# Kernel optimization log

Measured on AMD Instinct MI355X. Metric: run time of the kernel, lower is better.

The kernel has to match this reference:

```python
import jax, jax.numpy as jnp
import numpy as np

B, T, N, NIN = 2, 10, 128, 6
K, H = 4, 128          # edge_types, n_hid
E = N * (N - 1)        # fully-connected, no self-loops


def _linear_init(key, out_f, in_f, bias=True):
    k1, k2 = jax.random.split(key)
    bound = 1.0 / np.sqrt(in_f)
    W = jax.random.uniform(k1, (out_f, in_f), jnp.float32, -bound, bound)
    if bias:
        b = jax.random.uniform(k2, (out_f,), jnp.float32, -bound, bound)
        return W, b
    return W


def setup_inputs() -> dict:
    key = jax.random.key(0)
    ks = jax.random.split(key, 20)
    # graph structure: one-hot receiver/sender matrices (NRI style)
    off_diag = np.ones((N, N), dtype=np.float32) - np.eye(N, dtype=np.float32)
    send_idx, recv_idx = np.where(off_diag)
    eye = np.eye(N, dtype=np.float32)
    rel_rec = jnp.asarray(eye[recv_idx])   # [E, N]
    rel_send = jnp.asarray(eye[send_idx])  # [E, N]

    data = jax.random.normal(ks[0], (B, T, N, NIN), jnp.float32)
    rel_type = jax.nn.softmax(jax.random.normal(ks[1], (B, E, K), jnp.float32), axis=-1)

    # per-edge-type message MLPs, stacked over edge type
    m1 = [_linear_init(ks[2 + i], H, 2 * H) for i in range(K)]
    m2 = [_linear_init(ks[6 + i], H, H) for i in range(K)]
    W_msg1 = jnp.stack([w for w, _ in m1]); b_msg1 = jnp.stack([b for _, b in m1])
    W_msg2 = jnp.stack([w for w, _ in m2]); b_msg2 = jnp.stack([b for _, b in m2])

    W_hr = _linear_init(ks[10], H, H, bias=False)
    W_hi = _linear_init(ks[11], H, H, bias=False)
    W_hh = _linear_init(ks[12], H, H, bias=False)
    W_ir, b_ir = _linear_init(ks[13], H, NIN)
    W_ii, b_ii = _linear_init(ks[14], H, NIN)
    W_in, b_in = _linear_init(ks[15], H, NIN)
    W_o1, b_o1 = _linear_init(ks[16], H, H)
    W_o2, b_o2 = _linear_init(ks[17], H, H)
    W_o3, b_o3 = _linear_init(ks[18], NIN, H)

    return dict(data=data, rel_type=rel_type, rel_rec=rel_rec, rel_send=rel_send,
                W_msg1=W_msg1, b_msg1=b_msg1, W_msg2=W_msg2, b_msg2=b_msg2,
                W_hr=W_hr, W_hi=W_hi, W_hh=W_hh,
                W_ir=W_ir, b_ir=b_ir, W_ii=W_ii, b_ii=b_ii, W_in=W_in, b_in=b_in,
                W_o1=W_o1, b_o1=b_o1, W_o2=W_o2, b_o2=b_o2, W_o3=W_o3, b_o3=b_o3)


def reference(data, rel_type, rel_rec, rel_send,
              W_msg1, b_msg1, W_msg2, b_msg2,
              W_hr, W_hi, W_hh,
              W_ir, b_ir, W_ii, b_ii, W_in, b_in,
              W_o1, b_o1, W_o2, b_o2, W_o3, b_o3):
    norm = float(K)  # skip_first=False -> all edge types, norm = edge_types
    rel_type_k = jnp.transpose(rel_type, (2, 0, 1))[..., None]  # [K, B, E, 1]

    def single_step(hidden, ins):
        # gather node hidden states to edges
        receivers = jnp.einsum('en,bnh->beh', rel_rec, hidden)
        senders = jnp.einsum('en,bnh->beh', rel_send, hidden)
        pre_msg = jnp.concatenate([receivers, senders], axis=-1)  # [B, E, 2H]
        # per-edge-type 2-layer tanh MLP, batched over edge types (dropout p=0)
        msg = jnp.tanh(jnp.einsum('bef,khf->kbeh', pre_msg, W_msg1) + b_msg1[:, None, None, :])
        msg = jnp.tanh(jnp.einsum('kbeh,kgh->kbeg', msg, W_msg2) + b_msg2[:, None, None, :])
        all_msgs = jnp.sum(msg * rel_type_k, axis=0) / norm      # [B, E, H]
        # scatter-aggregate edge messages to receiver nodes
        agg = jnp.einsum('beh,en->bnh', all_msgs, rel_rec) / NIN  # [B, N, H]
        # GRU-style update
        r = jax.nn.sigmoid(ins @ W_ir.T + b_ir + agg @ W_hr.T)
        i = jax.nn.sigmoid(ins @ W_ii.T + b_ii + agg @ W_hi.T)
        n = jnp.tanh(ins @ W_in.T + b_in + r * (agg @ W_hh.T))
        hidden_new = (1.0 - i) * n + i * hidden
        # output MLP with residual (dropout p=0)
        p = jax.nn.relu(hidden_new @ W_o1.T + b_o1)
        p = jax.nn.relu(p @ W_o2.T + b_o2)
        pred = ins + p @ W_o3.T + b_o3
        return hidden_new, pred

    hidden0 = jnp.zeros((B, N, H), data.dtype)
    # pred_steps=1 (default) -> every step consumes the ground-truth frame
    ins_seq = jnp.transpose(data[:, :-1], (1, 0, 2, 3))  # [T-1, B, N, NIN]
    _, preds = jax.lax.scan(single_step, hidden0, ins_seq)
    # stack(dim=1).transpose(1,2) -> [B, N, T-1, NIN]
    return jnp.transpose(preds, (1, 2, 0, 3))
```

## Files before the change

### kernel.cpp

```cpp
#include <hip/hip_runtime.h>

#define NN 128
#define HH 128
#define BB 2
#define KT 4
#define EE 16256
#define TT 9

typedef __bf16 v8bf __attribute__((ext_vector_type(8)));
typedef float v4f __attribute__((ext_vector_type(4)));

__device__ __forceinline__ float tanh_fast(float x) {
  return 1.0f - __fdividef(2.0f, __expf(2.0f * x) + 1.0f);
}
__device__ __forceinline__ float sigmoid_fast(float x) {
  return __fdividef(1.0f, 1.0f + __expf(-x));
}
__device__ __forceinline__ unsigned short f2bf(float f) {
  unsigned int u = __float_as_uint(f);
  u += 0x7FFFu + ((u >> 16) & 1u);
  return (unsigned short)(u >> 16);
}

__global__ void prep_kernel(const float* __restrict__ W_msg1,
                            const float* __restrict__ W_msg2,
                            const float* __restrict__ rel_type,
                            unsigned short* __restrict__ W1hi,
                            unsigned short* __restrict__ W1lo,
                            unsigned short* __restrict__ W2bf,
                            float* __restrict__ relp) {
  int idx = blockIdx.x * 256 + threadIdx.x;
  {
    int h = idx & 127, g = (idx >> 7) & 127, ku = idx >> 14;
    int k = ku >> 1, u = ku & 1;
    float w = W_msg1[(k * 128 + g) * 256 + u * 128 + h];
    unsigned short hi = f2bf(w);
    float whi = __uint_as_float(((unsigned int)hi) << 16);
    W1hi[idx] = hi;
    W1lo[idx] = f2bf(w - whi);
  }
  if (idx < 65536) W2bf[idx] = f2bf(W_msg2[idx]);
  {
    int r = idx & 127, k = (idx >> 7) & 3, n = (idx >> 9) & 127, b = idx >> 16;
    float v = 0.f;
    if (r != n) {
      int e = r * 127 + (n < r ? n : n - 1);
      v = rel_type[(b * EE + e) * KT + k];
    }
    relp[idx] = v;
  }
}

__global__ __launch_bounds__(512)
void step_kernel(const float* __restrict__ data,
                 const float* __restrict__ b_msg1,
                 const float* __restrict__ b_msg2,
                 const float* __restrict__ W_hr,
                 const float* __restrict__ W_hi_,
                 const float* __restrict__ W_hh,
                 const float* __restrict__ W_ir, const float* __restrict__ b_ir,
                 const float* __restrict__ W_ii, const float* __restrict__ b_ii,
                 const float* __restrict__ W_in, const float* __restrict__ b_in,
                 const float* __restrict__ W_o1, const float* __restrict__ b_o1,
                 const float* __restrict__ W_o2, const float* __restrict__ b_o2,
                 const float* __restrict__ W_o3, const float* __restrict__ b_o3,
                 const unsigned short* __restrict__ W1hi,
                 const unsigned short* __restrict__ W1lo,
                 const unsigned short* __restrict__ W2bf,
                 const float* __restrict__ relp,
                 float* __restrict__ hidden,
                 const float* __restrict__ UVin,
                 float* __restrict__ UVout,
                 float* __restrict__ outp,
                 int t) {
  __shared__ unsigned short w2_lds[65536];
  __shared__ float ub_lds[512];
  __shared__ float b2_lds[512];
  __shared__ float rel_lds[512];
  __shared__ float colsum[8][128];
  __shared__ float agg_lds[128];
  __shared__ float hid_lds[128];
  __shared__ float hn_lds[128];
  __shared__ float ins_lds[6];
  __shared__ float g_r[128], g_i[128], g_hh[128], g_in[128];
  __shared__ float p1_lds[128], p2_lds[128];

  const int tid = threadIdx.x;
  const int lane = tid & 63;
  const int wave = tid >> 6;
  const int b = blockIdx.x >> 7;
  const int n = blockIdx.x & 127;

  {
    const uint4* w2g = (const uint4*)W2bf;
#pragma unroll
    for (int i = 0; i < 16; ++i) {
      int cid = tid + i * 512;
      int plane = cid >> 11, c2 = cid & 2047;
      int g = c2 >> 4, cc = c2 & 15;
      uint4 v = w2g[cid];
      int off = (plane << 15) + (g << 8) + (cc << 4);
      off ^= (g & 7) << 4;
      *(uint4*)((char*)w2_lds + off) = v;
    }
    int k = tid >> 7, h = tid & 127;
    ub_lds[tid] = UVin[(((k * 2 + 0) * BB + b) * NN + n) * HH + h] + b_msg1[tid];
    b2_lds[tid] = b_msg2[tid];
    rel_lds[tid] = relp[(b * NN + n) * (KT * NN) + tid];
  }
  __syncthreads();

  float acc_all[8][4];
#pragma unroll
  for (int c = 0; c < 8; ++c)
#pragma unroll
    for (int r = 0; r < 4; ++r) acc_all[c][r] = 0.f;

  for (int k = 0; k < KT; ++k) {
    const float* vbase = UVin + (((k * 2 + 1) * BB + b) * NN + (wave * 16 + (lane & 15))) * HH;
    v8bf af[4];
#pragma unroll
    for (int ks = 0; ks < 4; ++ks) {
      int c0 = ks * 32 + ((lane >> 4) << 3);
      float4 v0 = *(const float4*)(vbase + c0);
      float4 v1 = *(const float4*)(vbase + c0 + 4);
      const float* up = ub_lds + k * 128 + c0;
      float4 u0 = *(const float4*)(up);
      float4 u1 = *(const float4*)(up + 4);
      af[ks][0] = (__bf16)tanh_fast(u0.x + v0.x);
      af[ks][1] = (__bf16)tanh_fast(u0.y + v0.y);
      af[ks][2] = (__bf16)tanh_fast(u0.z + v0.z);
      af[ks][3] = (__bf16)tanh_fast(u0.w + v0.w);
      af[ks][4] = (__bf16)tanh_fast(u1.x + v1.x);
      af[ks][5] = (__bf16)tanh_fast(u1.y + v1.y);
      af[ks][6] = (__bf16)tanh_fast(u1.z + v1.z);
      af[ks][7] = (__bf16)tanh_fast(u1.w + v1.w);
    }
    v4f acck[8];
#pragma unroll
    for (int c = 0; c < 8; ++c) acck[c] = (v4f){0.f, 0.f, 0.f, 0.f};
#pragma unroll
    for (int ks = 0; ks < 4; ++ks) {
#pragma unroll
      for (int c = 0; c < 8; ++c) {
        int g = c * 16 + (lane & 15);
        int boff = (k << 15) + (g << 8) + (ks << 6) + ((lane >> 4) << 4);
        boff ^= (g & 7) << 4;
        v8bf bfrag = *(const v8bf*)((const char*)w2_lds + boff);
        acck[c] = __builtin_amdgcn_mfma_f32_16x16x32_bf16(af[ks], bfrag, acck[c], 0, 0, 0);
      }
    }
#pragma unroll
    for (int c = 0; c < 8; ++c) {
      float bb = b2_lds[k * 128 + c * 16 + (lane & 15)];
#pragma unroll
      for (int rg = 0; rg < 4; ++rg) {
        int rowg = wave * 16 + ((lane >> 4) << 2) + rg;
        acc_all[c][rg] += tanh_fast(acck[c][rg] + bb) * rel_lds[k * 128 + rowg];
      }
    }
  }

#pragma unroll
  for (int c = 0; c < 8; ++c) {
    float s = acc_all[c][0] + acc_all[c][1] + acc_all[c][2] + acc_all[c][3];
    s += __shfl_xor(s, 16);
    s += __shfl_xor(s, 32);
    if ((lane >> 4) == 0) colsum[wave][c * 16 + lane] = s;
  }
  __syncthreads();
  if (tid < 128) {
    float s = 0.f;
#pragma unroll
    for (int w = 0; w < 8; ++w) s += colsum[w][tid];
    agg_lds[tid] = s * (1.0f / 24.0f);
    hid_lds[tid] = hidden[(b * NN + n) * HH + tid];
  }
  if (tid >= 128 && tid < 134) ins_lds[tid - 128] = data[((b * 10 + t) * NN + n) * 6 + (tid - 128)];
  __syncthreads();

  {
    int h = tid >> 2, q = tid & 3;
    const float4* whr = (const float4*)(W_hr + h * 128 + q * 32);
    const float4* whi = (const float4*)(W_hi_ + h * 128 + q * 32);
    const float4* whh = (const float4*)(W_hh + h * 128 + q * 32);
    const float4* ag4 = (const float4*)(agg_lds + q * 32);
    float phr = 0.f, phi = 0.f, phh = 0.f;
#pragma unroll
    for (int j = 0; j < 8; ++j) {
      float4 a = ag4[j];
      float4 wr = whr[j], wi = whi[j], wh = whh[j];
      phr += wr.x * a.x + wr.y * a.y + wr.z * a.z + wr.w * a.w;
      phi += wi.x * a.x + wi.y * a.y + wi.z * a.z + wi.w * a.w;
      phh += wh.x * a.x + wh.y * a.y + wh.z * a.z + wh.w * a.w;
    }
    phr += __shfl_xor(phr, 1); phr += __shfl_xor(phr, 2);
    phi += __shfl_xor(phi, 1); phi += __shfl_xor(phi, 2);
    phh += __shfl_xor(phh, 1); phh += __shfl_xor(phh, 2);
    if (q == 0) {
      float dr = b_ir[h], di = b_ii[h], dn = b_in[h];
#pragma unroll
      for (int j = 0; j < 6; ++j) {
        float iv = ins_lds[j];
        dr += W_ir[h * 6 + j] * iv;
        di += W_ii[h * 6 + j] * iv;
        dn += W_in[h * 6 + j] * iv;
      }
      g_r[h] = dr + phr; g_i[h] = di + phi; g_hh[h] = phh; g_in[h] = dn;
    }
  }
  __syncthreads();
  if (tid < 128) {
    float r = sigmoid_fast(g_r[tid]);
    float ii = sigmoid_fast(g_i[tid]);
    float ng = tanh_fast(g_in[tid] + r * g_hh[tid]);
    float hn = (1.0f - ii) * ng + ii * hid_lds[tid];
    hn_lds[tid] = hn;
    hidden[(b * NN + n) * HH + tid] = hn;
  }
  __syncthreads();

  {
    int h = tid >> 2, q = tid & 3;
    const float4* w4 = (const float4*)(W_o1 + h * 128 + q * 32);
    const float4* a4 = (const float4*)(hn_lds + q * 32);
    float p = 0.f;
#pragma unroll
    for (int j = 0; j < 8; ++j) {
      float4 w = w4[j]; float4 a = a4[j];
      p += w.x * a.x + w.y * a.y + w.z * a.z + w.w * a.w;
    }
    p += __shfl_xor(p, 1); p += __shfl_xor(p, 2);
    if (q == 0) p1_lds[h] = fmaxf(p + b_o1[h], 0.f);
  }
  __syncthreads();
  {
    int h = tid >> 2, q = tid & 3;
    const float4* w4 = (const float4*)(W_o2 + h * 128 + q * 32);
    const float4* a4 = (const float4*)(p1_lds + q * 32);
    float p = 0.f;
#pragma unroll
    for (int j = 0; j < 8; ++j) {
      float4 w = w4[j]; float4 a = a4[j];
      p += w.x * a.x + w.y * a.y + w.z * a.z + w.w * a.w;
    }
    p += __shfl_xor(p, 1); p += __shfl_xor(p, 2);
    if (q == 0) p2_lds[h] = fmaxf(p + b_o2[h], 0.f);
  }
  __syncthreads();
  if (tid < 48) {
    int i = tid >> 3, oc = tid & 7;
    const float4* w4 = (const float4*)(W_o3 + i * 128 + oc * 16);
    const float4* a4 = (const float4*)(p2_lds + oc * 16);
    float p = 0.f;
#pragma unroll
    for (int j = 0; j < 4; ++j) {
      float4 w = w4[j]; float4 a = a4[j];
      p += w.x * a.x + w.y * a.y + w.z * a.z + w.w * a.w;
    }
    p += __shfl_xor(p, 1); p += __shfl_xor(p, 2); p += __shfl_xor(p, 4);
    if (oc == 0) outp[((b * NN + n) * TT + t) * 6 + i] = ins_lds[i] + p + b_o3[i];
  }

  {
    v8bf hf_hi[4], hf_lo[4];
#pragma unroll
    for (int q = 0; q < 4; ++q) {
      int c0 = q * 32 + ((lane >> 4) << 3);
      bool live = (lane & 15) == 0;
#pragma unroll
      for (int j = 0; j < 8; ++j) {
        float a = live ? hn_lds[c0 + j] : 0.f;
        __bf16 ah = (__bf16)a;
        hf_hi[q][j] = ah;
        hf_lo[q][j] = (__bf16)(a - (float)ah);
      }
    }
#pragma unroll
    for (int c = 0; c < 8; ++c) {
      int gg = (wave * 8 + c) * 16 + (lane & 15);
      v4f acc = (v4f){0.f, 0.f, 0.f, 0.f};
#pragma unroll
      for (int q = 0; q < 4; ++q) {
        int hoff = q * 32 + ((lane >> 4) << 3);
        v8bf bhi = *(const v8bf*)(W1hi + (size_t)gg * 128 + hoff);
        v8bf blo = *(const v8bf*)(W1lo + (size_t)gg * 128 + hoff);
        acc = __builtin_amdgcn_mfma_f32_16x16x32_bf16(hf_hi[q], bhi, acc, 0, 0, 0);
        acc = __builtin_amdgcn_mfma_f32_16x16x32_bf16(hf_lo[q], bhi, acc, 0, 0, 0);
        acc = __builtin_amdgcn_mfma_f32_16x16x32_bf16(hf_hi[q], blo, acc, 0, 0, 0);
      }
      if ((lane >> 4) == 0) {
        int kh = gg >> 7, g = gg & 127;
        UVout[((kh * BB + b) * NN + n) * HH + g] = acc[0];
      }
    }
  }
}

extern "C" void kernel_launch(void* const* d_in, const int* in_sizes, int n_in,
                              void* d_out, int out_size, void* d_ws, size_t ws_size,
                              hipStream_t stream) {
  const float* data     = (const float*)d_in[0];
  const float* rel_type = (const float*)d_in[1];
  const float* W_msg1 = (const float*)d_in[4];
  const float* b_msg1 = (const float*)d_in[5];
  const float* W_msg2 = (const float*)d_in[6];
  const float* b_msg2 = (const float*)d_in[7];
  const float* W_hr = (const float*)d_in[8];
  const float* W_hi = (const float*)d_in[9];
  const float* W_hh = (const float*)d_in[10];
  const float* W_ir = (const float*)d_in[11];
  const float* b_ir = (const float*)d_in[12];
  const float* W_ii = (const float*)d_in[13];
  const float* b_ii = (const float*)d_in[14];
  const float* W_in = (const float*)d_in[15];
  const float* b_in = (const float*)d_in[16];
  const float* W_o1 = (const float*)d_in[17];
  const float* b_o1 = (const float*)d_in[18];
  const float* W_o2 = (const float*)d_in[19];
  const float* b_o2 = (const float*)d_in[20];
  const float* W_o3 = (const float*)d_in[21];
  const float* b_o3 = (const float*)d_in[22];
  float* outp = (float*)d_out;

  char* ws = (char*)d_ws;
  float* hidden        = (float*)(ws);
  float* UVa           = (float*)(ws + 131072);
  float* UVb           = (float*)(ws + 1179648);
  unsigned short* W1hi = (unsigned short*)(ws + 2228224);
  unsigned short* W1lo = (unsigned short*)(ws + 2490368);
  unsigned short* W2bf = (unsigned short*)(ws + 2752512);
  float* relp          = (float*)(ws + 2883584);

  hipMemsetAsync(hidden, 0, 131072, stream);
  hipMemsetAsync(UVa, 0, 1048576, stream);
  prep_kernel<<<512, 256, 0, stream>>>(W_msg1, W_msg2, rel_type, W1hi, W1lo, W2bf, relp);

  for (int t = 0; t < TT; ++t) {
    float* uvin = (t & 1) ? UVb : UVa;
    float* uvout = (t & 1) ? UVa : UVb;
    step_kernel<<<BB * NN, 512, 0, stream>>>(
        data, b_msg1, b_msg2, W_hr, W_hi, W_hh,
        W_ir, b_ir, W_ii, b_ii, W_in, b_in,
        W_o1, b_o1, W_o2, b_o2, W_o3, b_o3,
        W1hi, W1lo, W2bf, relp, hidden, uvin, uvout, outp, t);
  }
}
```

Before: 583.0 us.

## Split step kernel into per-edge-type message kernel and GRU tail kernel

The fused per-node step kernel is split into two kernels. msg_kernel runs one block per (batch, node, edge type), so 1024 blocks of 256 threads each load only 32KB of W2 into LDS instead of 128KB, and each wave handles two row tiles that share every B fragment. Each block adds its partial aggregation into a per-timestep buffer with atomicAdd. tail_kernel then reads that buffer and does the GRU and output MLP. This is meant to raise occupancy and parallelism in the message GEMM, at the cost of an extra launch per step, float atomics (so summation order is no longer deterministic), and a global round-trip for the aggregate.

```diff
diff --git a/kernel.cpp b/kernel.cpp
--- a/kernel.cpp
+++ b/kernel.cpp
@@ -51,10 +51,112 @@
   }
 }
 
+__global__ __launch_bounds__(256)
+void msg_kernel(const float* __restrict__ b_msg1,
+                const float* __restrict__ b_msg2,
+                const unsigned short* __restrict__ W2bf,
+                const float* __restrict__ relp,
+                const float* __restrict__ UVin,
+                float* __restrict__ agg,
+                int dummy) {
+  __shared__ unsigned short w2_lds[16384];
+  __shared__ float ub_lds[128];
+  __shared__ float b2_lds[128];
+  __shared__ float rel_lds[128];
+  __shared__ float colsum[4][128];
+
+  const int tid = threadIdx.x;
+  const int lane = tid & 63;
+  const int wave = tid >> 6;
+  const int bid = blockIdx.x;
+  const int k = bid & 3;
+  const int n = (bid >> 2) & 127;
+  const int b = bid >> 9;
+
+  {
+    const uint4* w2g = (const uint4*)(W2bf + k * 16384);
+#pragma unroll
+    for (int i = 0; i < 8; ++i) {
+      int cid = tid + i * 256;
+      int g = cid >> 4, cc = cid & 15;
+      uint4 v = w2g[cid];
+      int off = (g << 8) + (cc << 4);
+      off ^= (g & 7) << 4;
+      *(uint4*)((char*)w2_lds + off) = v;
+    }
+    if (tid < 128) {
+      ub_lds[tid] = UVin[(((k * 2 + 0) * BB + b) * NN + n) * HH + tid] + b_msg1[k * 128 + tid];
+      b2_lds[tid] = b_msg2[k * 128 + tid];
+      rel_lds[tid] = relp[(b * NN + n) * (KT * NN) + k * 128 + tid];
+    }
+  }
+  __syncthreads();
+
+  v8bf af[2][4];
+#pragma unroll
+  for (int rt = 0; rt < 2; ++rt) {
+    int row = wave * 32 + rt * 16 + (lane & 15);
+    const float* vbase = UVin + (((k * 2 + 1) * BB + b) * NN + row) * HH;
+#pragma unroll
+    for (int ks = 0; ks < 4; ++ks) {
+      int c0 = ks * 32 + ((lane >> 4) << 3);
+      float4 v0 = *(const float4*)(vbase + c0);
+      float4 v1 = *(const float4*)(vbase + c0 + 4);
+      const float* up = ub_lds + c0;
+      af[rt][ks][0] = (__bf16)tanh_fast(up[0] + v0.x);
+      af[rt][ks][1] = (__bf16)tanh_fast(up[1] + v0.y);
+      af[rt][ks][2] = (__bf16)tanh_fast(up[2] + v0.z);
+      af[rt][ks][3] = (__bf16)tanh_fast(up[3] + v0.w);
+      af[rt][ks][4] = (__bf16)tanh_fast(up[4] + v1.x);
+      af[rt][ks][5] = (__bf16)tanh_fast(up[5] + v1.y);
+      af[rt][ks][6] = (__bf16)tanh_fast(up[6] + v1.z);
+      af[rt][ks][7] = (__bf16)tanh_fast(up[7] + v1.w);
+    }
+  }
+
+  v4f acck[2][8];
+#pragma unroll
+  for (int rt = 0; rt < 2; ++rt)
+#pragma unroll
+    for (int c = 0; c < 8; ++c) acck[rt][c] = (v4f){0.f, 0.f, 0.f, 0.f};
+#pragma unroll
+  for (int ks = 0; ks < 4; ++ks) {
+#pragma unroll
+    for (int c = 0; c < 8; ++c) {
+      int g = c * 16 + (lane & 15);
+      int boff = (g << 8) + (ks << 6) + ((lane >> 4) << 4);
+      boff ^= (g & 7) << 4;
+      v8bf bfrag = *(const v8bf*)((const char*)w2_lds + boff);
+      acck[0][c] = __builtin_amdgcn_mfma_f32_16x16x32_bf16(af[0][ks], bfrag, acck[0][c], 0, 0, 0);
+      acck[1][c] = __builtin_amdgcn_mfma_f32_16x16x32_bf16(af[1][ks], bfrag, acck[1][c], 0, 0, 0);
+    }
+  }
+
+#pragma unroll
+  for (int c = 0; c < 8; ++c) {
+    float bb = b2_lds[c * 16 + (lane & 15)];
+    float s = 0.f;
+#pragma unroll
+    for (int rt = 0; rt < 2; ++rt) {
+#pragma unroll
+      for (int rg = 0; rg < 4; ++rg) {
+        int row = wave * 32 + rt * 16 + ((lane >> 4) << 2) + rg;
+        s += tanh_fast(acck[rt][c][rg] + bb) * rel_lds[row];
+      }
+    }
+    s += __shfl_xor(s, 16);
+    s += __shfl_xor(s, 32);
+    if ((lane >> 4) == 0) colsum[wave][c * 16 + lane] = s;
+  }
+  __syncthreads();
+  if (tid < 128) {
+    float s = colsum[0][tid] + colsum[1][tid] + colsum[2][tid] + colsum[3][tid];
+    atomicAdd(agg + (b * NN + n) * HH + tid, s * (1.0f / 24.0f));
+  }
+}
+
 __global__ __launch_bounds__(512)
-void step_kernel(const float* __restrict__ data,
-                 const float* __restrict__ b_msg1,
-                 const float* __restrict__ b_msg2,
+void tail_kernel(const float* __restrict__ data,
                  const float* __restrict__ W_hr,
                  const float* __restrict__ W_hi_,
                  const float* __restrict__ W_hh,
@@ -66,18 +168,11 @@
                  const float* __restrict__ W_o3, const float* __restrict__ b_o3,
                  const unsigned short* __restrict__ W1hi,
                  const unsigned short* __restrict__ W1lo,
-                 const unsigned short* __restrict__ W2bf,
-                 const float* __restrict__ relp,
+                 const float* __restrict__ aggIn,
                  float* __restrict__ hidden,
-                 const float* __restrict__ UVin,
                  float* __restrict__ UVout,
                  float* __restrict__ outp,
                  int t) {
-  __shared__ unsigned short w2_lds[65536];
-  __shared__ float ub_lds[512];
-  __shared__ float b2_lds[512];
-  __shared__ float rel_lds[512];
-  __shared__ float colsum[8][128];
   __shared__ float agg_lds[128];
   __shared__ float hid_lds[128];
   __shared__ float hn_lds[128];
@@ -91,89 +186,8 @@
   const int b = blockIdx.x >> 7;
   const int n = blockIdx.x & 127;
 
-  {
-    const uint4* w2g = (const uint4*)W2bf;
-#pragma unroll
-    for (int i = 0; i < 16; ++i) {
-      int cid = tid + i * 512;
-      int plane = cid >> 11, c2 = cid & 2047;
-      int g = c2 >> 4, cc = c2 & 15;
-      uint4 v = w2g[cid];
-      int off = (plane << 15) + (g << 8) + (cc << 4);
-      off ^= (g & 7) << 4;
-      *(uint4*)((char*)w2_lds + off) = v;
-    }
-    int k = tid >> 7, h = tid & 127;
-    ub_lds[tid] = UVin[(((k * 2 + 0) * BB + b) * NN + n) * HH + h] + b_msg1[tid];
-    b2_lds[tid] = b_msg2[tid];
-    rel_lds[tid] = relp[(b * NN + n) * (KT * NN) + tid];
-  }
-  __syncthreads();
-
-  float acc_all[8][4];
-#pragma unroll
-  for (int c = 0; c < 8; ++c)
-#pragma unroll
-    for (int r = 0; r < 4; ++r) acc_all[c][r] = 0.f;
-
-  for (int k = 0; k < KT; ++k) {
-    const float* vbase = UVin + (((k * 2 + 1) * BB + b) * NN + (wave * 16 + (lane & 15))) * HH;
-    v8bf af[4];
-#pragma unroll
-    for (int ks = 0; ks < 4; ++ks) {
-      int c0 = ks * 32 + ((lane >> 4) << 3);
-      float4 v0 = *(const float4*)(vbase + c0);
-      float4 v1 = *(const float4*)(vbase + c0 + 4);
-      const float* up = ub_lds + k * 128 + c0;
-      float4 u0 = *(const float4*)(up);
-      float4 u1 = *(const float4*)(up + 4);
-      af[ks][0] = (__bf16)tanh_fast(u0.x + v0.x);
-      af[ks][1] = (__bf16)tanh_fast(u0.y + v0.y);
-      af[ks][2] = (__bf16)tanh_fast(u0.z + v0.z);
-      af[ks][3] = (__bf16)tanh_fast(u0.w + v0.w);
-      af[ks][4] = (__bf16)tanh_fast(u1.x + v1.x);
-      af[ks][5] = (__bf16)tanh_fast(u1.y + v1.y);
-      af[ks][6] = (__bf16)tanh_fast(u1.z + v1.z);
-      af[ks][7] = (__bf16)tanh_fast(u1.w + v1.w);
-    }
-    v4f acck[8];
-#pragma unroll
-    for (int c = 0; c < 8; ++c) acck[c] = (v4f){0.f, 0.f, 0.f, 0.f};
-#pragma unroll
-    for (int ks = 0; ks < 4; ++ks) {
-#pragma unroll
-      for (int c = 0; c < 8; ++c) {
-        int g = c * 16 + (lane & 15);
-        int boff = (k << 15) + (g << 8) + (ks << 6) + ((lane >> 4) << 4);
-        boff ^= (g & 7) << 4;
-        v8bf bfrag = *(const v8bf*)((const char*)w2_lds + boff);
-        acck[c] = __builtin_amdgcn_mfma_f32_16x16x32_bf16(af[ks], bfrag, acck[c], 0, 0, 0);
-      }
-    }
-#pragma unroll
-    for (int c = 0; c < 8; ++c) {
-      float bb = b2_lds[k * 128 + c * 16 + (lane & 15)];
-#pragma unroll
-      for (int rg = 0; rg < 4; ++rg) {
-        int rowg = wave * 16 + ((lane >> 4) << 2) + rg;
-        acc_all[c][rg] += tanh_fast(acck[c][rg] + bb) * rel_lds[k * 128 + rowg];
-      }
-    }
-  }
-
-#pragma unroll
-  for (int c = 0; c < 8; ++c) {
-    float s = acc_all[c][0] + acc_all[c][1] + acc_all[c][2] + acc_all[c][3];
-    s += __shfl_xor(s, 16);
-    s += __shfl_xor(s, 32);
-    if ((lane >> 4) == 0) colsum[wave][c * 16 + lane] = s;
-  }
-  __syncthreads();
   if (tid < 128) {
-    float s = 0.f;
-#pragma unroll
-    for (int w = 0; w < 8; ++w) s += colsum[w][tid];
-    agg_lds[tid] = s * (1.0f / 24.0f);
+    agg_lds[tid] = aggIn[(b * NN + n) * HH + tid];
     hid_lds[tid] = hidden[(b * NN + n) * HH + tid];
   }
   if (tid >= 128 && tid < 134) ins_lds[tid - 128] = data[((b * 10 + t) * NN + n) * 6 + (tid - 128)];
@@ -331,18 +345,22 @@
   unsigned short* W1lo = (unsigned short*)(ws + 2490368);
   unsigned short* W2bf = (unsigned short*)(ws + 2752512);
   float* relp          = (float*)(ws + 2883584);
+  float* aggbuf        = (float*)(ws + 3407872);
 
   hipMemsetAsync(hidden, 0, 131072, stream);
   hipMemsetAsync(UVa, 0, 1048576, stream);
+  hipMemsetAsync(aggbuf, 0, TT * 131072, stream);
   prep_kernel<<<512, 256, 0, stream>>>(W_msg1, W_msg2, rel_type, W1hi, W1lo, W2bf, relp);
 
   for (int t = 0; t < TT; ++t) {
     float* uvin = (t & 1) ? UVb : UVa;
     float* uvout = (t & 1) ? UVa : UVb;
-    step_kernel<<<BB * NN, 512, 0, stream>>>(
-        data, b_msg1, b_msg2, W_hr, W_hi, W_hh,
+    float* agg_t = aggbuf + t * (BB * NN * HH);
+    msg_kernel<<<BB * NN * KT, 256, 0, stream>>>(b_msg1, b_msg2, W2bf, relp, uvin, agg_t, 0);
+    tail_kernel<<<BB * NN, 512, 0, stream>>>(
+        data, W_hr, W_hi, W_hh,
         W_ir, b_ir, W_ii, b_ii, W_in, b_in,
         W_o1, b_o1, W_o2, b_o2, W_o3, b_o3,
-        W1hi, W1lo, W2bf, relp, hidden, uvin, uvout, outp, t);
-  }
-}
+        W1hi, W1lo, agg_t, hidden, uvout, outp, t);
+  }
+}
```

Measured after the change: 610.2 us. 4.7% more time.
